# Optimization experiments

Hardware: AMD Instinct MI355X
Metric: run time of the kernel (lower is better)

Reference implementation:

```python
import jax, jax.numpy as jnp
import numpy as np

N_NODES = 50000
N_EDGES = 800000
F_IN = 128
H1 = 100
H2 = 200
F_OUT = 16


def gcn_layer(x, W, b, row, col, n_nodes):
    """PyG GCNConv: x@W, add self-loops, symmetric deg normalization, scatter-add, +bias."""
    x = x @ W  # [N, out]
    # add self loops
    loop = jnp.arange(n_nodes, dtype=row.dtype)
    row_sl = jnp.concatenate([row, loop])
    col_sl = jnp.concatenate([col, loop])
    # degree over target index (col), incl. self loops
    deg = jax.ops.segment_sum(jnp.ones_like(col_sl, dtype=x.dtype), col_sl, num_segments=n_nodes)
    dis = jnp.where(deg > 0, jax.lax.rsqrt(deg), 0.0)  # deg^-0.5, inf->0
    norm = dis[row_sl] * dis[col_sl]  # [E+N]
    msg = x[row_sl] * norm[:, None]  # gather + scale, [E+N, out]
    out = jax.ops.segment_sum(msg, col_sl, num_segments=n_nodes)  # scatter-add
    return out + b


def setup_inputs() -> dict:
    key = jax.random.key(0)
    ks = jax.random.split(key, 9)
    x = jax.random.normal(ks[0], (N_NODES, F_IN), dtype=jnp.float32)
    edge_index = jax.random.randint(ks[1], (2, N_EDGES), 0, N_NODES, dtype=jnp.int64)
    s1 = 1.0 / np.sqrt(F_IN)
    s2 = 1.0 / np.sqrt(H1)
    s3 = 1.0 / np.sqrt(H2)
    W1 = jax.random.uniform(ks[2], (F_IN, H1), jnp.float32, -s1, s1)
    b1 = jnp.zeros((H1,), jnp.float32)
    W2 = jax.random.uniform(ks[3], (H1, H2), jnp.float32, -s2, s2)
    b2 = jnp.zeros((H2,), jnp.float32)
    Wfc = jax.random.uniform(ks[4], (H2, F_OUT), jnp.float32, -s3, s3)
    bfc = jax.random.uniform(ks[5], (F_OUT,), jnp.float32, -s3, s3)
    return {"edge_features": x, "edge_indices": edge_index,
            "W1": W1, "b1": b1, "W2": W2, "b2": b2, "Wfc": Wfc, "bfc": bfc}


def reference(edge_features, edge_indices, W1, b1, W2, b2, Wfc, bfc):
    row, col = edge_indices[0], edge_indices[1]
    x = gcn_layer(edge_features, W1, b1, row, col, N_NODES)
    x = jax.nn.relu(x)
    x = gcn_layer(x, W2, b2, row, col, N_NODES)
    x = jax.nn.relu(x)
    return x @ Wfc + bfc
```

## Files before the change

kernel.cpp:

```cpp
#include <hip/hip_runtime.h>
#include <hip/hip_fp16.h>

#define N_NODES 50000
#define N_EDGES 800000
#define F_IN 128
#define H1 100
#define H2 200
#define F_OUT 16
#define CAP 64
#define NXCD 8
#define DRANGE (N_NODES / NXCD)

typedef _Float16 f16x8 __attribute__((ext_vector_type(8)));
typedef _Float16 f16x4 __attribute__((ext_vector_type(4)));
typedef float f32x4 __attribute__((ext_vector_type(4)));


__global__ void count_fill_kernel(const int* __restrict__ col, const int* __restrict__ row,
                                  int* __restrict__ cnt, unsigned short* __restrict__ csrf,
                                  int n_edges, int chunk) {
    int d = blockIdx.x & 7;
    int lo = d * DRANGE, hi = lo + DRANGE;
    int base = (int)(blockIdx.x >> 3) * chunk;
    int end = min(base + chunk, n_edges);
    for (int e = base + threadIdx.x; e < end; e += blockDim.x) {
        int c = col[e];
        if (c >= lo && c < hi) {
            int r = atomicAdd(&cnt[c], 1);
            if (r < CAP) csrf[(size_t)c * CAP + r] = (unsigned short)row[e];
        }
    }
}


__global__ __launch_bounds__(256) void gemm1_kernel(
        const float* __restrict__ A, const float* __restrict__ W,
        const int* __restrict__ cnt, _Float16* __restrict__ out, int n_rows) {
    constexpr int BM = 128, BK = 32, PIT = 40, K = F_IN, LDW = H1;
    __shared__ _Float16 As[BM * PIT];
    __shared__ _Float16 Bs[112 * PIT];

    int tid = threadIdx.x;
    int w = tid >> 6, lane = tid & 63;
    int lrow = lane & 15, lk = lane >> 4;
    int m0 = blockIdx.x * BM;

    f32x4 acc[2][7];
#pragma unroll
    for (int m = 0; m < 2; ++m)
#pragma unroll
        for (int nf = 0; nf < 7; ++nf) acc[m][nf] = (f32x4){0.f, 0.f, 0.f, 0.f};

    for (int kc = 0; kc < K; kc += BK) {
        __syncthreads();
        for (int i = tid; i < BM * 8; i += 256) {
            int r = i >> 3, q = i & 7;
            float4 v = make_float4(0.f, 0.f, 0.f, 0.f);
            if (m0 + r < n_rows) v = *(const float4*)&A[(size_t)(m0 + r) * K + kc + q * 4];
            f16x4 h = {(_Float16)v.x, (_Float16)v.y, (_Float16)v.z, (_Float16)v.w};
            *(f16x4*)&As[r * PIT + q * 4] = h;
        }
        for (int i = tid; i < 112 * BK; i += 256) {
            int k = i / 112, c = i - k * 112;
            float v = (c < LDW) ? W[(size_t)(kc + k) * LDW + c] : 0.f;
            Bs[c * PIT + k] = (_Float16)v;
        }
        __syncthreads();
        f16x8 a0 = *(const f16x8*)&As[(w * 32 + lrow) * PIT + lk * 8];
        f16x8 a1 = *(const f16x8*)&As[(w * 32 + 16 + lrow) * PIT + lk * 8];
#pragma unroll
        for (int nf = 0; nf < 7; ++nf) {
            f16x8 b = *(const f16x8*)&Bs[(nf * 16 + lrow) * PIT + lk * 8];
            acc[0][nf] = __builtin_amdgcn_mfma_f32_16x16x32_f16(a0, b, acc[0][nf], 0, 0, 0);
            acc[1][nf] = __builtin_amdgcn_mfma_f32_16x16x32_f16(a1, b, acc[1][nf], 0, 0, 0);
        }
    }

#pragma unroll
    for (int m = 0; m < 2; ++m) {
        int rb = m0 + w * 32 + m * 16 + lk * 4;
#pragma unroll
        for (int r = 0; r < 4; ++r) {
            int grow = rb + r;
            if (grow >= n_rows) continue;
            float d = rsqrtf((float)cnt[grow] + 1.0f);
            size_t base = (size_t)grow * 104;
#pragma unroll
            for (int nf = 0; nf < 7; ++nf) {
                int c = nf * 16 + lrow;
                if (c < 100) out[base + c] = (_Float16)(acc[m][nf][r] * d);
            }
        }
    }
}


__global__ __launch_bounds__(256) void gemm2_kernel(
        const _Float16* __restrict__ A, const float* __restrict__ W,
        const float* __restrict__ b2, _Float16* __restrict__ out,
        size_t planeH, int n_rows) {
    constexpr int BM = 128, BK = 32, PIT = 40, K = H1, LDW = H2;
    __shared__ _Float16 As[BM * PIT];
    __shared__ _Float16 Bs[112 * PIT];

    int tid = threadIdx.x;
    int w = tid >> 6, lane = tid & 63;
    int lrow = lane & 15, lk = lane >> 4;
    int m0 = blockIdx.x * BM;
    int col_off = blockIdx.y * 100;

    f32x4 acc[2][7];
#pragma unroll
    for (int m = 0; m < 2; ++m)
#pragma unroll
        for (int nf = 0; nf < 7; ++nf) acc[m][nf] = (f32x4){0.f, 0.f, 0.f, 0.f};

    for (int kc = 0; kc < K; kc += BK) {
        __syncthreads();
        for (int i = tid; i < BM * 8; i += 256) {
            int r = i >> 3, q = i & 7, kb = kc + q * 4;
            f16x4 h = {(_Float16)0.f, (_Float16)0.f, (_Float16)0.f, (_Float16)0.f};
            if (m0 + r < n_rows && kb < K)
                h = *(const f16x4*)&A[(size_t)(m0 + r) * 104 + kb];
            *(f16x4*)&As[r * PIT + q * 4] = h;
        }
        for (int i = tid; i < 112 * BK; i += 256) {
            int k = i / 112, c = i - k * 112;
            float v = (c < 100 && kc + k < K) ? W[(size_t)(kc + k) * LDW + col_off + c] : 0.f;
            Bs[c * PIT + k] = (_Float16)v;
        }
        __syncthreads();
        f16x8 a0 = *(const f16x8*)&As[(w * 32 + lrow) * PIT + lk * 8];
        f16x8 a1 = *(const f16x8*)&As[(w * 32 + 16 + lrow) * PIT + lk * 8];
#pragma unroll
        for (int nf = 0; nf < 7; ++nf) {
            f16x8 b = *(const f16x8*)&Bs[(nf * 16 + lrow) * PIT + lk * 8];
            acc[0][nf] = __builtin_amdgcn_mfma_f32_16x16x32_f16(a0, b, acc[0][nf], 0, 0, 0);
            acc[1][nf] = __builtin_amdgcn_mfma_f32_16x16x32_f16(a1, b, acc[1][nf], 0, 0, 0);
        }
    }

    _Float16* o = out + blockIdx.y * planeH;
    float bv[7];
#pragma unroll
    for (int nf = 0; nf < 7; ++nf) {
        int c = nf * 16 + lrow;
        bv[nf] = (c < 100) ? b2[col_off + c] : 0.f;
    }
#pragma unroll
    for (int m = 0; m < 2; ++m) {
        int rb = m0 + w * 32 + m * 16 + lk * 4;
#pragma unroll
        for (int r = 0; r < 4; ++r) {
            int grow = rb + r;
            if (grow >= n_rows) continue;
            size_t base = (size_t)grow * 104;
#pragma unroll
            for (int nf = 0; nf < 7; ++nf) {
                int c = nf * 16 + lrow;
                if (c < 100) o[base + c] = (_Float16)fmaxf(acc[m][nf][r] + bv[nf], 0.f);
            }
        }
    }
}


template <bool L1>
__global__ void agg_h_kernel(const __half2* __restrict__ Y, const int* __restrict__ cnt,
                             const unsigned short* __restrict__ csrf,
                             const float* __restrict__ bias,
                             __half2* __restrict__ out, int n_nodes) {
    int wave = threadIdx.x >> 6, lane = threadIdx.x & 63;
    int n = blockIdx.x * 4 + wave;
    if (n >= n_nodes) return;
    bool act = lane < 50;
    float ax = 0.f, ay = 0.f;
    if (act) {
        float2 v = __half22float2(Y[(size_t)n * 52 + lane]);
        ax = v.x; ay = v.y;
    }
    int deg0 = cnt[n];
    int deg = min(deg0, CAP);
    const unsigned short* slots = csrf + (size_t)n * CAP;
    int my = (lane < deg) ? (int)slots[lane] : 0;
    int i = 0;
    for (; i + 8 <= deg; i += 8) {
        int s0 = __shfl(my, i),     s1 = __shfl(my, i + 1);
        int s2 = __shfl(my, i + 2), s3 = __shfl(my, i + 3);
        int s4 = __shfl(my, i + 4), s5 = __shfl(my, i + 5);
        int s6 = __shfl(my, i + 6), s7 = __shfl(my, i + 7);
        if (act) {
            float2 v0 = __half22float2(Y[(size_t)s0 * 52 + lane]);
            float2 v1 = __half22float2(Y[(size_t)s1 * 52 + lane]);
            float2 v2 = __half22float2(Y[(size_t)s2 * 52 + lane]);
            float2 v3 = __half22float2(Y[(size_t)s3 * 52 + lane]);
            float2 v4 = __half22float2(Y[(size_t)s4 * 52 + lane]);
            float2 v5 = __half22float2(Y[(size_t)s5 * 52 + lane]);
            float2 v6 = __half22float2(Y[(size_t)s6 * 52 + lane]);
            float2 v7 = __half22float2(Y[(size_t)s7 * 52 + lane]);
            ax += ((v0.x + v1.x) + (v2.x + v3.x)) + ((v4.x + v5.x) + (v6.x + v7.x));
            ay += ((v0.y + v1.y) + (v2.y + v3.y)) + ((v4.y + v5.y) + (v6.y + v7.y));
        }
    }
    for (; i + 4 <= deg; i += 4) {
        int s0 = __shfl(my, i),     s1 = __shfl(my, i + 1);
        int s2 = __shfl(my, i + 2), s3 = __shfl(my, i + 3);
        if (act) {
            float2 v0 = __half22float2(Y[(size_t)s0 * 52 + lane]);
            float2 v1 = __half22float2(Y[(size_t)s1 * 52 + lane]);
            float2 v2 = __half22float2(Y[(size_t)s2 * 52 + lane]);
            float2 v3 = __half22float2(Y[(size_t)s3 * 52 + lane]);
            ax += (v0.x + v1.x) + (v2.x + v3.x);
            ay += (v0.y + v1.y) + (v2.y + v3.y);
        }
    }
    for (; i < deg; ++i) {
        int s = __shfl(my, i);
        if (act) {
            float2 v = __half22float2(Y[(size_t)s * 52 + lane]);
            ax += v.x; ay += v.y;
        }
    }
    if (act) {
        float d = rsqrtf((float)deg0 + 1.0f);
        float ox, oy;
        if (L1) {
            int f = lane * 2;
            ox = fmaxf(fmaf(ax, d, bias[f]), 0.f) * d;
            oy = fmaxf(fmaf(ay, d, bias[f + 1]), 0.f) * d;
        } else {
            ox = ax * d;
            oy = ay * d;
        }
        out[(size_t)n * 52 + lane] = __float22half2_rn(make_float2(ox, oy));
    }
}


__global__ void fc_h_kernel(const __half2* __restrict__ h2, size_t plane2,
                            const float* __restrict__ W, const float* __restrict__ b,
                            float* __restrict__ out, int n_rows) {
    int idx = blockIdx.x * blockDim.x + threadIdx.x;
    int n = idx >> 2;
    int cg = (idx & 3) * 4;
    if (n >= n_rows) return;
    float a0 = 0.f, a1 = 0.f, a2 = 0.f, a3 = 0.f;
#pragma unroll
    for (int p = 0; p < 2; ++p) {
        const __half2* hr = h2 + p * plane2 + (size_t)n * 52;
        const float* Wp = W + (size_t)(p * 100) * F_OUT + cg;
#pragma unroll 5
        for (int k2 = 0; k2 < 50; ++k2) {
            float2 hv = __half22float2(hr[k2]);
            float4 w0 = *(const float4*)&Wp[(2 * k2) * F_OUT];
            float4 w1 = *(const float4*)&Wp[(2 * k2 + 1) * F_OUT];
            a0 = fmaf(hv.x, w0.x, fmaf(hv.y, w1.x, a0));
            a1 = fmaf(hv.x, w0.y, fmaf(hv.y, w1.y, a1));
            a2 = fmaf(hv.x, w0.z, fmaf(hv.y, w1.z, a2));
            a3 = fmaf(hv.x, w0.w, fmaf(hv.y, w1.w, a3));
        }
    }
    float4 bv = *(const float4*)&b[cg];
    float4 o = {a0 + bv.x, a1 + bv.y, a2 + bv.z, a3 + bv.w};
    *(float4*)&out[(size_t)n * F_OUT + cg] = o;
}


extern "C" void kernel_launch(void* const* d_in, const int* in_sizes, int n_in,
                              void* d_out, int out_size, void* d_ws, size_t ws_size,
                              hipStream_t stream) {
    const float* x   = (const float*)d_in[0];
    const int*   ei  = (const int*)d_in[1];
    const float* W1  = (const float*)d_in[2];
    const float* b1  = (const float*)d_in[3];
    const float* W2  = (const float*)d_in[4];
    const float* b2  = (const float*)d_in[5];
    const float* Wfc = (const float*)d_in[6];
    const float* bfc = (const float*)d_in[7];
    float* out = (float*)d_out;

    const int N = N_NODES, E = N_EDGES;
    const int* row = ei;
    const int* col = ei + E;

    char* ws = (char*)d_ws;
    int*            cnt  = (int*)ws;             ws += (size_t)N * 4;
    unsigned short* csrf = (unsigned short*)ws;  ws += (size_t)N * CAP * 2;
    _Float16*       y1s  = (_Float16*)ws;        ws += (size_t)N * 104 * 2;
    _Float16*       h1s  = (_Float16*)ws;        ws += (size_t)N * 104 * 2;
    _Float16*       g2h  = (_Float16*)ws;        ws += (size_t)N * 104 * 2;
    _Float16*       h2   = y1s;

    hipMemsetAsync(cnt, 0, (size_t)N * 4, stream);

    const int NCHUNK = 392;
    const int CHUNK = (E + NCHUNK - 1) / NCHUNK;
    count_fill_kernel<<<NCHUNK * NXCD, 256, 0, stream>>>(col, row, cnt, csrf, E, CHUNK);

    const int GX = (N + 127) / 128;

    gemm1_kernel<<<GX, 256, 0, stream>>>(x, W1, cnt, y1s, N);
    agg_h_kernel<true><<<N / 4, 256, 0, stream>>>((const __half2*)y1s, cnt, csrf, b1, (__half2*)h1s, N);

    agg_h_kernel<false><<<N / 4, 256, 0, stream>>>((const __half2*)h1s, cnt, csrf, nullptr, (__half2*)g2h, N);
    gemm2_kernel<<<dim3(GX, 2), 256, 0, stream>>>(g2h, W2, b2, h2, (size_t)N * 104, N);

    fc_h_kernel<<<(N * 4 + 255) / 256, 256, 0, stream>>>((const __half2*)h2, (size_t)N * 52, Wfc, bfc, out, N);
}
```

Baseline: 270.4 us.

## Use XCC-aware dynamic ticket scheduling in CSR count/fill kernel

Instead of assuming blockIdx.x & 7 maps to an XCD, each block reads its hardware XCC ID and takes edge chunks from a per-destination-range ticket counter. Each XCD then handles the destination nodes that belong to its own partition, so cnt/csrf atomics stay local to that XCD's L2. Blocks that finish their own range steal chunks from the other ranges. The cost is a global ticket atomic plus two block barriers per chunk, and a fixed 2048-block persistent grid.

```diff
diff --git a/kernel.cpp b/kernel.cpp
--- a/kernel.cpp
+++ b/kernel.cpp
@@ -18,16 +18,30 @@
 
 __global__ void count_fill_kernel(const int* __restrict__ col, const int* __restrict__ row,
                                   int* __restrict__ cnt, unsigned short* __restrict__ csrf,
-                                  int n_edges, int chunk) {
-    int d = blockIdx.x & 7;
-    int lo = d * DRANGE, hi = lo + DRANGE;
-    int base = (int)(blockIdx.x >> 3) * chunk;
-    int end = min(base + chunk, n_edges);
-    for (int e = base + threadIdx.x; e < end; e += blockDim.x) {
-        int c = col[e];
-        if (c >= lo && c < hi) {
-            int r = atomicAdd(&cnt[c], 1);
-            if (r < CAP) csrf[(size_t)c * CAP + r] = (unsigned short)row[e];
+                                  int* __restrict__ tickets,
+                                  int n_edges, int chunk, int nchunk) {
+    unsigned xcc;
+    asm volatile("s_getreg_b32 %0, hwreg(HW_REG_XCC_ID)" : "=s"(xcc));
+    int d = (int)(xcc & 7);
+    __shared__ int s_t;
+    for (int dd = 0; dd < NXCD; ++dd) {
+        int q = (d + dd) & 7;
+        int lo = q * DRANGE, hi = lo + DRANGE;
+        for (;;) {
+            if (threadIdx.x == 0) s_t = atomicAdd(&tickets[q], 1);
+            __syncthreads();
+            int t = s_t;
+            __syncthreads();
+            if (t >= nchunk) break;
+            int base = t * chunk;
+            int end = min(base + chunk, n_edges);
+            for (int e = base + (int)threadIdx.x; e < end; e += blockDim.x) {
+                int c = col[e];
+                if (c >= lo && c < hi) {
+                    int r = atomicAdd(&cnt[c], 1);
+                    if (r < CAP) csrf[(size_t)c * CAP + r] = (unsigned short)row[e];
+                }
+            }
         }
     }
 }
@@ -284,18 +298,19 @@
     const int* col = ei + E;
 
     char* ws = (char*)d_ws;
-    int*            cnt  = (int*)ws;             ws += (size_t)N * 4;
-    unsigned short* csrf = (unsigned short*)ws;  ws += (size_t)N * CAP * 2;
-    _Float16*       y1s  = (_Float16*)ws;        ws += (size_t)N * 104 * 2;
-    _Float16*       h1s  = (_Float16*)ws;        ws += (size_t)N * 104 * 2;
-    _Float16*       g2h  = (_Float16*)ws;        ws += (size_t)N * 104 * 2;
-    _Float16*       h2   = y1s;
-
-    hipMemsetAsync(cnt, 0, (size_t)N * 4, stream);
-
-    const int NCHUNK = 392;
-    const int CHUNK = (E + NCHUNK - 1) / NCHUNK;
-    count_fill_kernel<<<NCHUNK * NXCD, 256, 0, stream>>>(col, row, cnt, csrf, E, CHUNK);
+    int*            cnt     = (int*)ws;             ws += (size_t)N * 4;
+    int*            tickets = (int*)ws;             ws += 64;
+    unsigned short* csrf    = (unsigned short*)ws;  ws += (size_t)N * CAP * 2;
+    _Float16*       y1s     = (_Float16*)ws;        ws += (size_t)N * 104 * 2;
+    _Float16*       h1s     = (_Float16*)ws;        ws += (size_t)N * 104 * 2;
+    _Float16*       g2h     = (_Float16*)ws;        ws += (size_t)N * 104 * 2;
+    _Float16*       h2      = y1s;
+
+    hipMemsetAsync(cnt, 0, (size_t)N * 4 + 64, stream);
+
+    const int CHUNK = 3200;
+    const int NCHUNK = (E + CHUNK - 1) / CHUNK;
+    count_fill_kernel<<<2048, 256, 0, stream>>>(col, row, cnt, csrf, tickets, E, CHUNK, NCHUNK);
 
     const int GX = (N + 127) / 128;
 
```

Result: slower. 466.0 us (+72.3%).

## Fuse CSR build into GEMM1 launch and move source-degree scaling into aggregation

Applied to the files above, without the earlier changes.

Merges the edge count/fill pass and the first GEMM into one launch, with the leading blocks doing edge insertion and the rest doing GEMM. Because GEMM1 can no longer read the degree counts, its output stays unscaled, and the first aggregation applies the source-degree normalization per neighbor using fma with shuffled degree factors. The goal is to remove a kernel boundary and let the scatter work overlap the GEMM. In exchange, the XCD-partitioned atomic scheme is dropped, the first aggregation does extra cnt gathers and shuffles, and its 4-wide unrolled tail loop is removed.

```diff
diff --git a/kernel.cpp b/kernel.cpp
--- a/kernel.cpp
+++ b/kernel.cpp
@@ -8,42 +8,35 @@
 #define H2 200
 #define F_OUT 16
 #define CAP 64
-#define NXCD 8
-#define DRANGE (N_NODES / NXCD)
 
 typedef _Float16 f16x8 __attribute__((ext_vector_type(8)));
 typedef _Float16 f16x4 __attribute__((ext_vector_type(4)));
 typedef float f32x4 __attribute__((ext_vector_type(4)));
 
 
-__global__ void count_fill_kernel(const int* __restrict__ col, const int* __restrict__ row,
-                                  int* __restrict__ cnt, unsigned short* __restrict__ csrf,
-                                  int n_edges, int chunk) {
-    int d = blockIdx.x & 7;
-    int lo = d * DRANGE, hi = lo + DRANGE;
-    int base = (int)(blockIdx.x >> 3) * chunk;
-    int end = min(base + chunk, n_edges);
-    for (int e = base + threadIdx.x; e < end; e += blockDim.x) {
-        int c = col[e];
-        if (c >= lo && c < hi) {
-            int r = atomicAdd(&cnt[c], 1);
-            if (r < CAP) csrf[(size_t)c * CAP + r] = (unsigned short)row[e];
-        }
-    }
-}
-
-
-__global__ __launch_bounds__(256) void gemm1_kernel(
+__global__ __launch_bounds__(256) void build_gemm1_kernel(
+        const int* __restrict__ col, const int* __restrict__ rowi,
+        int* __restrict__ cnt, unsigned short* __restrict__ csrf,
         const float* __restrict__ A, const float* __restrict__ W,
-        const int* __restrict__ cnt, _Float16* __restrict__ out, int n_rows) {
+        _Float16* __restrict__ out, int n_edges, int ncf, int n_rows) {
     constexpr int BM = 128, BK = 32, PIT = 40, K = F_IN, LDW = H1;
     __shared__ _Float16 As[BM * PIT];
     __shared__ _Float16 Bs[112 * PIT];
 
+    if (blockIdx.x < ncf) {
+        int e = blockIdx.x * 256 + threadIdx.x;
+        if (e < n_edges) {
+            int c = col[e];
+            int r = atomicAdd(&cnt[c], 1);
+            if (r < CAP) csrf[(size_t)c * CAP + r] = (unsigned short)rowi[e];
+        }
+        return;
+    }
+
     int tid = threadIdx.x;
     int w = tid >> 6, lane = tid & 63;
     int lrow = lane & 15, lk = lane >> 4;
-    int m0 = blockIdx.x * BM;
+    int m0 = (blockIdx.x - ncf) * BM;
 
     f32x4 acc[2][7];
 #pragma unroll
@@ -83,12 +76,11 @@
         for (int r = 0; r < 4; ++r) {
             int grow = rb + r;
             if (grow >= n_rows) continue;
-            float d = rsqrtf((float)cnt[grow] + 1.0f);
             size_t base = (size_t)grow * 104;
 #pragma unroll
             for (int nf = 0; nf < 7; ++nf) {
                 int c = nf * 16 + lrow;
-                if (c < 100) out[base + c] = (_Float16)(acc[m][nf][r] * d);
+                if (c < 100) out[base + c] = (_Float16)acc[m][nf][r];
             }
         }
     }
@@ -165,7 +157,7 @@
 }
 
 
-template <bool L1>
+template <bool SCALE_SRC>
 __global__ void agg_h_kernel(const __half2* __restrict__ Y, const int* __restrict__ cnt,
                              const unsigned short* __restrict__ csrf,
                              const float* __restrict__ bias,
@@ -174,21 +166,34 @@
     int n = blockIdx.x * 4 + wave;
     if (n >= n_nodes) return;
     bool act = lane < 50;
+    int deg0 = cnt[n];
+    int deg = min(deg0, CAP);
+    float dn = rsqrtf((float)deg0 + 1.0f);
+
     float ax = 0.f, ay = 0.f;
     if (act) {
         float2 v = __half22float2(Y[(size_t)n * 52 + lane]);
-        ax = v.x; ay = v.y;
-    }
-    int deg0 = cnt[n];
-    int deg = min(deg0, CAP);
+        float sc = SCALE_SRC ? dn : 1.0f;
+        ax = sc * v.x; ay = sc * v.y;
+    }
     const unsigned short* slots = csrf + (size_t)n * CAP;
     int my = (lane < deg) ? (int)slots[lane] : 0;
+    float dv = 1.0f;
+    if (SCALE_SRC) dv = rsqrtf((float)cnt[my] + 1.0f);
+
     int i = 0;
     for (; i + 8 <= deg; i += 8) {
         int s0 = __shfl(my, i),     s1 = __shfl(my, i + 1);
         int s2 = __shfl(my, i + 2), s3 = __shfl(my, i + 3);
         int s4 = __shfl(my, i + 4), s5 = __shfl(my, i + 5);
         int s6 = __shfl(my, i + 6), s7 = __shfl(my, i + 7);
+        float d0 = 1.f, d1 = 1.f, d2 = 1.f, d3 = 1.f, d4 = 1.f, d5 = 1.f, d6 = 1.f, d7 = 1.f;
+        if (SCALE_SRC) {
+            d0 = __shfl(dv, i);     d1 = __shfl(dv, i + 1);
+            d2 = __shfl(dv, i + 2); d3 = __shfl(dv, i + 3);
+            d4 = __shfl(dv, i + 4); d5 = __shfl(dv, i + 5);
+            d6 = __shfl(dv, i + 6); d7 = __shfl(dv, i + 7);
+        }
         if (act) {
             float2 v0 = __half22float2(Y[(size_t)s0 * 52 + lane]);
             float2 v1 = __half22float2(Y[(size_t)s1 * 52 + lane]);
@@ -198,39 +203,35 @@
             float2 v5 = __half22float2(Y[(size_t)s5 * 52 + lane]);
             float2 v6 = __half22float2(Y[(size_t)s6 * 52 + lane]);
             float2 v7 = __half22float2(Y[(size_t)s7 * 52 + lane]);
-            ax += ((v0.x + v1.x) + (v2.x + v3.x)) + ((v4.x + v5.x) + (v6.x + v7.x));
-            ay += ((v0.y + v1.y) + (v2.y + v3.y)) + ((v4.y + v5.y) + (v6.y + v7.y));
-        }
-    }
-    for (; i + 4 <= deg; i += 4) {
-        int s0 = __shfl(my, i),     s1 = __shfl(my, i + 1);
-        int s2 = __shfl(my, i + 2), s3 = __shfl(my, i + 3);
-        if (act) {
-            float2 v0 = __half22float2(Y[(size_t)s0 * 52 + lane]);
-            float2 v1 = __half22float2(Y[(size_t)s1 * 52 + lane]);
-            float2 v2 = __half22float2(Y[(size_t)s2 * 52 + lane]);
-            float2 v3 = __half22float2(Y[(size_t)s3 * 52 + lane]);
-            ax += (v0.x + v1.x) + (v2.x + v3.x);
-            ay += (v0.y + v1.y) + (v2.y + v3.y);
+            if (SCALE_SRC) {
+                ax = fmaf(d0, v0.x, fmaf(d1, v1.x, fmaf(d2, v2.x, fmaf(d3, v3.x, ax))));
+                ax = fmaf(d4, v4.x, fmaf(d5, v5.x, fmaf(d6, v6.x, fmaf(d7, v7.x, ax))));
+                ay = fmaf(d0, v0.y, fmaf(d1, v1.y, fmaf(d2, v2.y, fmaf(d3, v3.y, ay))));
+                ay = fmaf(d4, v4.y, fmaf(d5, v5.y, fmaf(d6, v6.y, fmaf(d7, v7.y, ay))));
+            } else {
+                ax += ((v0.x + v1.x) + (v2.x + v3.x)) + ((v4.x + v5.x) + (v6.x + v7.x));
+                ay += ((v0.y + v1.y) + (v2.y + v3.y)) + ((v4.y + v5.y) + (v6.y + v7.y));
+            }
         }
     }
     for (; i < deg; ++i) {
         int s = __shfl(my, i);
+        float ds = SCALE_SRC ? __shfl(dv, i) : 1.0f;
         if (act) {
             float2 v = __half22float2(Y[(size_t)s * 52 + lane]);
-            ax += v.x; ay += v.y;
+            if (SCALE_SRC) { ax = fmaf(ds, v.x, ax); ay = fmaf(ds, v.y, ay); }
+            else           { ax += v.x; ay += v.y; }
         }
     }
     if (act) {
-        float d = rsqrtf((float)deg0 + 1.0f);
         float ox, oy;
-        if (L1) {
+        if (SCALE_SRC) {
             int f = lane * 2;
-            ox = fmaxf(fmaf(ax, d, bias[f]), 0.f) * d;
-            oy = fmaxf(fmaf(ay, d, bias[f + 1]), 0.f) * d;
+            ox = fmaxf(fmaf(ax, dn, bias[f]), 0.f) * dn;
+            oy = fmaxf(fmaf(ay, dn, bias[f + 1]), 0.f) * dn;
         } else {
-            ox = ax * d;
-            oy = ay * d;
+            ox = ax * dn;
+            oy = ay * dn;
         }
         out[(size_t)n * 52 + lane] = __float22half2_rn(make_float2(ox, oy));
     }
@@ -286,24 +287,22 @@
     char* ws = (char*)d_ws;
     int*            cnt  = (int*)ws;             ws += (size_t)N * 4;
     unsigned short* csrf = (unsigned short*)ws;  ws += (size_t)N * CAP * 2;
-    _Float16*       y1s  = (_Float16*)ws;        ws += (size_t)N * 104 * 2;
+    _Float16*       y1u  = (_Float16*)ws;        ws += (size_t)N * 104 * 2;
     _Float16*       h1s  = (_Float16*)ws;        ws += (size_t)N * 104 * 2;
     _Float16*       g2h  = (_Float16*)ws;        ws += (size_t)N * 104 * 2;
-    _Float16*       h2   = y1s;
+    _Float16*       h2   = y1u;
 
     hipMemsetAsync(cnt, 0, (size_t)N * 4, stream);
 
-    const int NCHUNK = 392;
-    const int CHUNK = (E + NCHUNK - 1) / NCHUNK;
-    count_fill_kernel<<<NCHUNK * NXCD, 256, 0, stream>>>(col, row, cnt, csrf, E, CHUNK);
-
+    const int NCF = (E + 255) / 256;
     const int GX = (N + 127) / 128;
 
-    gemm1_kernel<<<GX, 256, 0, stream>>>(x, W1, cnt, y1s, N);
-    agg_h_kernel<true><<<N / 4, 256, 0, stream>>>((const __half2*)y1s, cnt, csrf, b1, (__half2*)h1s, N);
+    build_gemm1_kernel<<<NCF + GX, 256, 0, stream>>>(col, row, cnt, csrf, x, W1, y1u, E, NCF, N);
+
+    agg_h_kernel<true><<<N / 4, 256, 0, stream>>>((const __half2*)y1u, cnt, csrf, b1, (__half2*)h1s, N);
 
     agg_h_kernel<false><<<N / 4, 256, 0, stream>>>((const __half2*)h1s, cnt, csrf, nullptr, (__half2*)g2h, N);
+
     gemm2_kernel<<<dim3(GX, 2), 256, 0, stream>>>(g2h, W2, b2, h2, (size_t)N * 104, N);
-
     fc_h_kernel<<<(N * 4 + 255) / 256, 256, 0, stream>>>((const __half2*)h2, (size_t)N * 52, Wfc, bfc, out, N);
 }
```

After: 291.3 us. 1.08x slower.
